# Optimization experiments

Hardware: AMD Instinct MI355X
Metric: run time of the kernel (lower is better)

## Reference

```python
import jax, jax.numpy as jnp
import numpy as np

K = 16          # n_neighbors
DS = 4          # downsampling_rate
EPS = 1e-5      # BatchNorm eps


def fps(pos, n_samples):
    """Farthest point sampling. pos: [N,3] -> [n_samples] int32 indices (start at node 0)."""
    N = pos.shape[0]
    def body(carry, _):
        dists, last = carry
        d = jnp.sum((pos - pos[last]) ** 2, axis=-1)
        dists = jnp.minimum(dists, d)
        nxt = jnp.argmax(dists).astype(jnp.int32)
        return (dists, nxt), nxt
    init = (jnp.full((N,), 1e10, dtype=pos.dtype), jnp.int32(0))
    _, idxs = jax.lax.scan(body, init, None, length=n_samples - 1)
    return jnp.concatenate([jnp.zeros((1,), jnp.int32), idxs])


def knn(pos, k):
    """k nearest neighbors (incl. self). pos: [N,3] -> [N,k] indices."""
    d = jnp.sum((pos[:, None, :] - pos[None, :, :]) ** 2, axis=-1)  # [N,N]
    _, idx = jax.lax.top_k(-d, k)
    return idx


def setup_inputs() -> dict:
    key = jax.random.key(0)
    ks = jax.random.split(key, 8)
    B, N, C = 4, 4096, 64
    sizes = [C + 3, 128, 128]
    inp = {
        "feat": jax.random.normal(ks[0], (B, N, C), jnp.float32),
        "pos": jax.random.normal(ks[1], (B, N, 3), jnp.float32),
    }
    for i in range(2):
        cin, cout = sizes[i], sizes[i + 1]
        inp[f"W{i+1}"] = jax.random.normal(ks[2 + 2 * i], (cout, cin), jnp.float32) / np.float32(np.sqrt(cin))
        inp[f"b{i+1}"] = jnp.zeros((cout,), jnp.float32)
        inp[f"gamma{i+1}"] = jnp.ones((cout,), jnp.float32)
        inp[f"beta{i+1}"] = jnp.zeros((cout,), jnp.float32)
    return inp


def reference(feat, pos, W1, b1, gamma1, beta1, W2, b2, gamma2, beta2):
    B, N, C = feat.shape
    n_samples = N // DS
    # FPS centroids; the torch code selects them via a boolean mask, i.e. ascending node order
    cent = jax.vmap(lambda p: fps(p, n_samples))(pos)          # [B,S]
    cent = jnp.sort(cent, axis=-1)
    # KNN graph per cloud
    nbr = jax.vmap(lambda p: knn(p, K))(pos)                    # [B,N,K]
    nbr_pos = jax.vmap(lambda p, i: p[i])(pos, nbr)             # [B,N,K,3]
    nbr_feat = jax.vmap(lambda f, i: f[i])(feat, nbr)           # [B,N,K,C]
    # RelativePositionMessage: concat(src_pos - dst_pos, src_feat)
    rel = nbr_pos - pos[:, :, None, :]
    h = jnp.concatenate([rel, nbr_feat], axis=-1)               # [B,N,K,C+3]
    # PointNetConv: (1x1 Conv2d -> BatchNorm2d(training stats) -> ReLU) x2, then max over neighbors
    for W, b, g, be in ((W1, b1, gamma1, beta1), (W2, b2, gamma2, beta2)):
        h = jnp.einsum('bnkc,dc->bnkd', h, W) + b
        mu = jnp.mean(h, axis=(0, 1, 2))
        var = jnp.var(h, axis=(0, 1, 2))
        h = (h - mu) * jax.lax.rsqrt(var + EPS) * g + be
        h = jax.nn.relu(h)
    new_feat = jnp.max(h, axis=2)                               # [B,N,Cout]
    # select centroid nodes
    pos_res = jnp.take_along_axis(pos, cent[..., None], axis=1)        # [B,S,3]
    feat_res = jnp.take_along_axis(new_feat, cent[..., None], axis=1)  # [B,S,Cout]
    return pos_res, feat_res
```

## Files before the change

### kernel.cpp

```cpp
#include <hip/hip_runtime.h>

typedef float f2 __attribute__((ext_vector_type(2)));

#define NB 4
#define NN 4096
#define KNB 16
#define NS 1024
#define M1TOT (NB*NN*KNB)
#define EPSBN 1e-5f
#define FPS_SPLIT 511
#define PADN 4124

__device__ __align__(16) float g_h1[(size_t)M1TOT*128];
__device__ __align__(16) int   g_nbr[NB*NN*KNB];
__device__ __align__(16) float g_fps_rd[NB][NN];
__device__ unsigned g_fps_sel[NB][256];
__device__ int   g_fps_last[NB];
__device__ int   g_cent[NB][NS];
__device__ float g_sum1[128], g_sq1[128], g_sum2[128], g_sq2[128];
__device__ __align__(16) float g_hminN[NB*NN*128];
__device__ __align__(16) float g_hmaxN[NB*NN*128];

struct __align__(16) FpsSm {
    float spx[NN], spy[NN], spz[NN];
    float sv[2][4]; int sj[2][4];
    int   cnts[256];
};
struct __align__(16) G1Sm {
    float  xls[64*68];
    float4 wlsA[68*16], wlsB[68*16];
    float  redS[512], redQ[512];
};
struct __align__(16) G2Sm {
    float  yls[64*132];
    float4 w2A[32*16], w2B[32*16];
    float  scs[128], shs[128];
    float  redS[512], redQ[512];
};
union KnnSm {
    struct { float spx[PADN], spy[PADN], spz[PADN]; } p;
    unsigned long long pairs[32*130];
};

__device__ __forceinline__ void fps_chunk(const float* __restrict__ pos, float* __restrict__ out,
                                          FpsSm* sm, int b, int t, int it0, int it1,
                                          bool first, bool last)
{
#pragma clang fp contract(off)
    const float* pb = pos + b*NN*3;
    for (int i = t; i < NN; i += 256) { sm->spx[i]=pb[3*i]; sm->spy[i]=pb[3*i+1]; sm->spz[i]=pb[3*i+2]; }
    __syncthreads();
    f2 rx[8], ry[8], rz[8], rd[8];
    #pragma unroll
    for (int p=0;p<8;p++){
        int j = (t<<4) + 2*p;
        rx[p] = *(const f2*)&sm->spx[j];
        ry[p] = *(const f2*)&sm->spy[j];
        rz[p] = *(const f2*)&sm->spz[j];
    }
    unsigned sel; int j2;
    if (first) {
        #pragma unroll
        for (int p=0;p<8;p++) rd[p] = (f2){1e10f, 1e10f};
        sel = (t==0) ? 1u : 0u;
        j2 = 0;
    } else {
        #pragma unroll
        for (int u=0;u<4;u++){
            float4 ld = *(const float4*)&g_fps_rd[b][(t<<4)+(u<<2)];
            rd[2*u]   = (f2){ld.x, ld.y};
            rd[2*u+1] = (f2){ld.z, ld.w};
        }
        sel = g_fps_sel[b][t];
        j2  = g_fps_last[b];
    }
    float cx = sm->spx[j2], cy = sm->spy[j2], cz = sm->spz[j2];

    for (int it = it0; it < it1; ++it) {
        const int par = it & 1;
        const f2 c2x = {cx,cx}, c2y = {cy,cy}, c2z = {cz,cz};
        #pragma unroll
        for (int p=0;p<8;p++){
            f2 dx = rx[p]-c2x, dy = ry[p]-c2y, dz = rz[p]-c2z;
            f2 m0 = dx*dx, m1 = dy*dy, m2 = dz*dz;
            f2 a0 = m0 + m1;
            f2 d  = a0 + m2;
            rd[p] = __builtin_elementwise_min(rd[p], d);
        }
        f2 t0 = __builtin_elementwise_max(rd[0], rd[1]);
        f2 t1 = __builtin_elementwise_max(rd[2], rd[3]);
        f2 t2 = __builtin_elementwise_max(rd[4], rd[5]);
        f2 t3 = __builtin_elementwise_max(rd[6], rd[7]);
        t0 = __builtin_elementwise_max(t0, t1);
        t2 = __builtin_elementwise_max(t2, t3);
        t0 = __builtin_elementwise_max(t0, t2);
        float wv = fmaxf(t0.x, t0.y);
        #pragma unroll
        for (int m=1;m<64;m<<=1) wv = fmaxf(wv, __shfl_xor(wv, m));
        int lj = 0x7fffffff;
        #pragma unroll
        for (int p=7;p>=0;p--){
            lj = (rd[p].y == wv) ? ((t<<4)+2*p+1) : lj;
            lj = (rd[p].x == wv) ? ((t<<4)+2*p)   : lj;
        }
        unsigned long long mk = __ballot(lj != 0x7fffffff);
        int src = __ffsll(mk) - 1;
        int bj = __shfl(lj, src);
        if ((t & 63) == 0) { sm->sv[par][t>>6] = wv; sm->sj[par][t>>6] = bj; }
        __syncthreads();
        float v = sm->sv[par][0]; int jn = sm->sj[par][0];
        #pragma unroll
        for (int w=1;w<4;w++){
            float ov = sm->sv[par][w]; int oj = sm->sj[par][w];
            if (ov > v || (ov == v && oj < jn)) { v = ov; jn = oj; }
        }
        j2 = jn;
        cx = sm->spx[j2]; cy = sm->spy[j2]; cz = sm->spz[j2];
        unsigned rel = (unsigned)(j2 - (t<<4));
        if (rel < 16u) sel |= (1u << rel);
    }

    if (!last) {
        #pragma unroll
        for (int u=0;u<4;u++){
            float4 st = {rd[2*u].x, rd[2*u].y, rd[2*u+1].x, rd[2*u+1].y};
            *(float4*)&g_fps_rd[b][(t<<4)+(u<<2)] = st;
        }
        g_fps_sel[b][t] = sel;
        if (t == 0) g_fps_last[b] = j2;
    } else {
        sm->cnts[t] = (int)__popc(sel);
        __syncthreads();
        if (t == 0) { int run = 0; for (int i=0;i<256;i++){ int c = sm->cnts[i]; sm->cnts[i] = run; run += c; } }
        __syncthreads();
        int base = sm->cnts[t];
        #pragma unroll
        for (int i=0;i<16;i++){
            int j = (t<<4)+i;
            if (sel & (1u<<i)) {
                g_cent[b][base] = j;
                float* po = out + (size_t)((b<<10)+base)*3;
                po[0]=sm->spx[j]; po[1]=sm->spy[j]; po[2]=sm->spz[j];
                base++;
            }
        }
    }
}

__device__ __forceinline__ void key_ins(unsigned long long (&kk)[16], unsigned long long &wmax,
                                        unsigned long long key)
{
    unsigned long long m0 = kk[0]; int mj = 0;
    #pragma unroll
    for (int u=1;u<16;u++){ if (kk[u] > m0){ m0 = kk[u]; mj = u; } }
    #pragma unroll
    for (int u=0;u<16;u++){ if (u == mj) kk[u] = key; }
    unsigned long long w = kk[0];
    #pragma unroll
    for (int u=1;u<16;u++) w = (kk[u] > w) ? kk[u] : w;
    wmax = w;
}

__global__ __launch_bounds__(256, 1) void kPre(const float* __restrict__ pos)
{
    __shared__ KnnSm sm;
    const int blk = blockIdx.x, t = threadIdx.x;
    if (blk >= 512) {
        if (t < 128) { g_sum1[t]=0.f; g_sq1[t]=0.f; g_sum2[t]=0.f; g_sq2[t]=0.f; }
        return;
    }
    const int b = blk >> 7;
    const int qloc = t >> 3, tq = t & 7;
    const int q = ((blk & 127) << 5) + qloc;
    const float* pb = pos + b*NN*3;
    for (int i = t; i < NN; i += 256) {
        int l = i + ((i >> 9) << 2);
        sm.p.spx[l]=pb[3*i]; sm.p.spy[l]=pb[3*i+1]; sm.p.spz[l]=pb[3*i+2];
    }
    __syncthreads();
    const int lq = q + ((q >> 9) << 2);
    const float qx = sm.p.spx[lq], qy = sm.p.spy[lq], qz = sm.p.spz[lq];
    float bd[16]; int bi[16];
    #pragma unroll
    for (int u=0;u<16;u++){ bd[u]=3e38f; bi[u]=0; }
    float wmax = 3e38f;
    const int base = tq * 516;
    const int j0 = tq << 9;
    for (int i = 0; i < 512; ++i) {
        float dx = sm.p.spx[base+i]-qx, dy = sm.p.spy[base+i]-qy, dz = sm.p.spz[base+i]-qz;
        float d = __fadd_rn(__fadd_rn(__fmul_rn(dx,dx),__fmul_rn(dy,dy)),__fmul_rn(dz,dz));
        if (d < wmax) {
            float m0 = bd[0]; int mj = 0;
            #pragma unroll
            for (int u=1;u<16;u++){ if (bd[u] > m0) { m0 = bd[u]; mj = u; } }
            #pragma unroll
            for (int u=0;u<16;u++){ if (u == mj) { bd[u] = d; bi[u] = j0 + i; } }
            wmax = bd[0];
            #pragma unroll
            for (int u=1;u<16;u++) wmax = fmaxf(wmax, bd[u]);
        }
    }
    __syncthreads();
    #pragma unroll
    for (int u=0;u<16;u++)
        sm.pairs[qloc*130 + (tq<<4) + u] =
            ((unsigned long long)__float_as_uint(bd[u]) << 32) | (unsigned)bi[u];
    __syncthreads();
    if (tq == 0) {
        unsigned long long kk2[16];
        #pragma unroll
        for (int u=0;u<16;u++) kk2[u] = ~0ULL;
        unsigned long long wm2 = ~0ULL;
        for (int e = 0; e < 128; ++e) {
            unsigned long long key = sm.pairs[qloc*130 + e];
            if (key < wm2) key_ins(kk2, wm2, key);
        }
        int* dst = g_nbr + ((size_t)(b*NN + q) << 4);
        #pragma unroll
        for (int u=0;u<16;u++) dst[u] = (int)(kk2[u] & 0xffffffffu);
    }
}

__global__ __launch_bounds__(256, 1) void kS1(const float* __restrict__ feat, const float* __restrict__ pos,
                                              const float* __restrict__ W1, const float* __restrict__ b1)
{
    __shared__ union { FpsSm f; G1Sm g; } sm;
    const int blk = blockIdx.x, t = threadIdx.x;
    if (blk < 4) { fps_chunk(pos, nullptr, &sm.f, blk, t, 0, FPS_SPLIT, true, false); return; }
    const int gb = blk - 4;
    const int b = gb >> 10, nb = (gb & 1023) << 2;

    for (int e = t; e < 128*67; e += 256) {
        int co = e / 67, ci = e - co*67;
        int row = (ci < 3) ? (64 + ci) : (ci - 3);
        int cgd = co >> 3, h = co & 7;
        float w = W1[e];
        if (h < 4) ((float*)&sm.g.wlsA[row*16 + cgd])[h]   = w;
        else       ((float*)&sm.g.wlsB[row*16 + cgd])[h-4] = w;
    }
    if (t < 64) { ((float*)&sm.g.wlsA[67*16])[t] = 0.f; ((float*)&sm.g.wlsB[67*16])[t] = 0.f; }
    {
        const int s = t >> 2, h = t & 3;
        const int n = nb + (s >> 4), k = s & 15;
        const int gq = b*NN + n;
        const int idx = g_nbr[(gq << 4) + k];
        const float* fr = feat + ((size_t)(b*NN + idx) << 6) + (h << 4);
        float* xr = sm.g.xls + s*68 + (h << 4);
        #pragma unroll
        for (int u=0;u<4;u++) ((float4*)xr)[u] = ((const float4*)fr)[u];
        if (h == 0) {
            const float* pn = pos + (size_t)gq*3;
            const float* pi = pos + (size_t)(b*NN + idx)*3;
            sm.g.xls[s*68 + 64] = pi[0]-pn[0];
            sm.g.xls[s*68 + 65] = pi[1]-pn[1];
            sm.g.xls[s*68 + 66] = pi[2]-pn[2];
            sm.g.xls[s*68 + 67] = 0.f;
        }
    }
    __syncthreads();
    const int cg = t & 15, sg = t >> 4, w = t >> 6;
    float acc[4][8];
    #pragma unroll
    for (int r=0;r<4;r++)
        #pragma unroll
        for (int c=0;c<8;c++) acc[r][c] = 0.f;
    for (int c4 = 0; c4 < 17; ++c4) {
        float4 wA[4], wB[4];
        #pragma unroll
        for (int ii=0;ii<4;ii++){ wA[ii] = sm.g.wlsA[(4*c4+ii)*16 + cg]; wB[ii] = sm.g.wlsB[(4*c4+ii)*16 + cg]; }
        #pragma unroll
        for (int r=0;r<4;r++){
            float4 xv = *(const float4*)&sm.g.xls[(sg + (r<<4))*68 + (c4<<2)];
            #pragma unroll
            for (int ii=0;ii<4;ii++){
                float x = (ii==0)?xv.x:(ii==1)?xv.y:(ii==2)?xv.z:xv.w;
                acc[r][0] = fmaf(x, wA[ii].x, acc[r][0]);
                acc[r][1] = fmaf(x, wA[ii].y, acc[r][1]);
                acc[r][2] = fmaf(x, wA[ii].z, acc[r][2]);
                acc[r][3] = fmaf(x, wA[ii].w, acc[r][3]);
                acc[r][4] = fmaf(x, wB[ii].x, acc[r][4]);
                acc[r][5] = fmaf(x, wB[ii].y, acc[r][5]);
                acc[r][6] = fmaf(x, wB[ii].z, acc[r][6]);
                acc[r][7] = fmaf(x, wB[ii].w, acc[r][7]);
            }
        }
    }
    float4 bA = *(const float4*)&b1[cg<<3];
    float4 bB = *(const float4*)&b1[(cg<<3)+4];
    float h1v[4][8];
    #pragma unroll
    for (int r=0;r<4;r++){
        h1v[r][0]=acc[r][0]+bA.x; h1v[r][1]=acc[r][1]+bA.y; h1v[r][2]=acc[r][2]+bA.z; h1v[r][3]=acc[r][3]+bA.w;
        h1v[r][4]=acc[r][4]+bB.x; h1v[r][5]=acc[r][5]+bB.y; h1v[r][6]=acc[r][6]+bB.z; h1v[r][7]=acc[r][7]+bB.w;
    }
    #pragma unroll
    for (int c=0;c<8;c++){
        const int ch = (cg<<3)+c;
        float ls=0.f, lq=0.f;
        #pragma unroll
        for (int r=0;r<4;r++){ float h1 = h1v[r][c]; ls += h1; lq = fmaf(h1,h1,lq); }
        ls += __shfl_xor(ls,16); ls += __shfl_xor(ls,32);
        lq += __shfl_xor(lq,16); lq += __shfl_xor(lq,32);
        if ((sg & 3) == 0) { sm.g.redS[w*128 + ch] = ls; sm.g.redQ[w*128 + ch] = lq; }
    }
    #pragma unroll
    for (int r=0;r<4;r++){
        const int gs = (b*NN + nb + r)*16 + sg;
        float4 o0 = {h1v[r][0],h1v[r][1],h1v[r][2],h1v[r][3]};
        float4 o1 = {h1v[r][4],h1v[r][5],h1v[r][6],h1v[r][7]};
        *(float4*)&g_h1[(size_t)gs*128 + (cg<<3)]     = o0;
        *(float4*)&g_h1[(size_t)gs*128 + (cg<<3) + 4] = o1;
    }
    __syncthreads();
    if (t < 128) {
        float s = sm.g.redS[t] + sm.g.redS[128+t] + sm.g.redS[256+t] + sm.g.redS[384+t];
        float q = sm.g.redQ[t] + sm.g.redQ[128+t] + sm.g.redQ[256+t] + sm.g.redQ[384+t];
        atomicAdd(&g_sum1[t], s);
        atomicAdd(&g_sq1[t], q);
    }
}

__global__ __launch_bounds__(256, 1) void kS2(const float* __restrict__ pos, float* __restrict__ out,
        const float* __restrict__ W2, const float* __restrict__ b2,
        const float* __restrict__ gamma1, const float* __restrict__ beta1)
{
    __shared__ union { FpsSm f; G2Sm g; } sm;
    const int blk = blockIdx.x, t = threadIdx.x;
    if (blk < 4) { fps_chunk(pos, out, &sm.f, blk, t, FPS_SPLIT, NS-1, false, true); return; }
    const int gb = blk - 4;
    const int b = gb >> 10, nb = (gb & 1023) << 2;
    if (t < 128) {
        const float inv = 1.f/(float)M1TOT;
        float mu  = g_sum1[t]*inv;
        float var = g_sq1[t]*inv - mu*mu;
        float sc  = gamma1[t]*rsqrtf(var + EPSBN);
        sm.g.scs[t] = sc; sm.g.shs[t] = beta1[t] - mu*sc;
    }
    __syncthreads();
    {
        const float* hsrc = g_h1 + (size_t)((b*NN + nb)*16)*128;
        const int ch0 = (4*t) & 127;
        float4 sc4 = *(const float4*)&sm.g.scs[ch0];
        float4 sh4 = *(const float4*)&sm.g.shs[ch0];
        #pragma unroll
        for (int j=0;j<8;j++){
            int f = j*1024 + 4*t;
            float4 v = *(const float4*)&hsrc[f];
            int s = f >> 7;
            float4 yv;
            yv.x = fmaxf(0.f, fmaf(v.x, sc4.x, sh4.x));
            yv.y = fmaxf(0.f, fmaf(v.y, sc4.y, sh4.y));
            yv.z = fmaxf(0.f, fmaf(v.z, sc4.z, sh4.z));
            yv.w = fmaxf(0.f, fmaf(v.w, sc4.w, sh4.w));
            *(float4*)&sm.g.yls[s*132 + ch0] = yv;
        }
    }
    const int cg = t & 15, sg = t >> 4, w = t >> 6;
    float acc2[4][8];
    #pragma unroll
    for (int r=0;r<4;r++)
        #pragma unroll
        for (int c=0;c<8;c++) acc2[r][c]=0.f;
    for (int kc = 0; kc < 4; ++kc) {
        for (int e = t; e < 4096; e += 256) {
            int d = e >> 5, kk = e & 31;
            float wv = W2[(d << 7) + (kc<<5) + kk];
            int cgd = d >> 3, h = d & 7;
            if (h < 4) ((float*)&sm.g.w2A[kk*16 + cgd])[h]   = wv;
            else       ((float*)&sm.g.w2B[kk*16 + cgd])[h-4] = wv;
        }
        __syncthreads();
        #pragma unroll
        for (int c4=0;c4<8;c4++){
            float4 wA[4], wB[4];
            #pragma unroll
            for (int ii=0;ii<4;ii++){ wA[ii] = sm.g.w2A[(4*c4+ii)*16 + cg]; wB[ii] = sm.g.w2B[(4*c4+ii)*16 + cg]; }
            #pragma unroll
            for (int r=0;r<4;r++){
                float4 yv = *(const float4*)&sm.g.yls[((sg<<2)+r)*132 + (kc<<5) + (c4<<2)];
                #pragma unroll
                for (int ii=0;ii<4;ii++){
                    float y = (ii==0)?yv.x:(ii==1)?yv.y:(ii==2)?yv.z:yv.w;
                    acc2[r][0] = fmaf(y, wA[ii].x, acc2[r][0]);
                    acc2[r][1] = fmaf(y, wA[ii].y, acc2[r][1]);
                    acc2[r][2] = fmaf(y, wA[ii].z, acc2[r][2]);
                    acc2[r][3] = fmaf(y, wA[ii].w, acc2[r][3]);
                    acc2[r][4] = fmaf(y, wB[ii].x, acc2[r][4]);
                    acc2[r][5] = fmaf(y, wB[ii].y, acc2[r][5]);
                    acc2[r][6] = fmaf(y, wB[ii].z, acc2[r][6]);
                    acc2[r][7] = fmaf(y, wB[ii].w, acc2[r][7]);
                }
            }
        }
        __syncthreads();
    }
    const int node = nb + (sg >> 2);
    #pragma unroll
    for (int c=0;c<8;c++){
        const int ch = (cg<<3)+c;
        const float bb = b2[ch];
        float ls=0.f, lq=0.f, mn=3e38f, mx=-3e38f;
        #pragma unroll
        for (int r=0;r<4;r++){
            float h2 = acc2[r][c] + bb;
            ls += h2; lq = fmaf(h2,h2,lq);
            mn = fminf(mn,h2); mx = fmaxf(mx,h2);
        }
        ls += __shfl_xor(ls,16); ls += __shfl_xor(ls,32);
        lq += __shfl_xor(lq,16); lq += __shfl_xor(lq,32);
        if ((sg & 3) == 0) { sm.g.redS[w*128 + ch] = ls; sm.g.redQ[w*128 + ch] = lq; }
        float o;
        o = __shfl_xor(mn,16); mn = fminf(mn,o);
        o = __shfl_xor(mn,32); mn = fminf(mn,o);
        o = __shfl_xor(mx,16); mx = fmaxf(mx,o);
        o = __shfl_xor(mx,32); mx = fmaxf(mx,o);
        if ((sg & 3) == 0) {
            const int oo = ((b<<12)+node)*128 + ch;
            g_hminN[oo] = mn; g_hmaxN[oo] = mx;
        }
    }
    __syncthreads();
    if (t < 128) {
        float s = sm.g.redS[t] + sm.g.redS[128+t] + sm.g.redS[256+t] + sm.g.redS[384+t];
        float q = sm.g.redQ[t] + sm.g.redQ[128+t] + sm.g.redQ[256+t] + sm.g.redQ[384+t];
        atomicAdd(&g_sum2[t], s);
        atomicAdd(&g_sq2[t], q);
    }
}

__global__ __launch_bounds__(256) void kFinal(const float* __restrict__ gamma2, const float* __restrict__ beta2,
                                              float* __restrict__ out)
{
    const int gid = blockIdx.x*256 + threadIdx.x;
    const int base = gid << 2;
    const int sl = base >> 7;
    const int b = sl >> 10, slot = sl & 1023;
    const int ch0 = base & 127;
    const int node = g_cent[b][slot];
    const int src = ((b<<12)+node)*128 + ch0;
    const float inv = 1.f/(float)M1TOT;
    float4 mx = *(const float4*)&g_hmaxN[src];
    float4 mn = *(const float4*)&g_hminN[src];
    float4 o;
    #pragma unroll
    for (int c=0;c<4;c++){
        int ch = ch0 + c;
        float mu = g_sum2[ch]*inv, var = g_sq2[ch]*inv - mu*mu;
        float sc = gamma2[ch]*rsqrtf(var+EPSBN), sh = beta2[ch] - mu*sc;
        float hi = (c==0)?mx.x:(c==1)?mx.y:(c==2)?mx.z:mx.w;
        float lo = (c==0)?mn.x:(c==1)?mn.y:(c==2)?mn.z:mn.w;
        float v = fmaxf(0.f, fmaf((sc >= 0.f) ? hi : lo, sc, sh));
        if (c==0) o.x=v; else if (c==1) o.y=v; else if (c==2) o.z=v; else o.w=v;
    }
    *(float4*)&out[12288 + base] = o;
}

extern "C" void kernel_launch(void* const* d_in, const int* in_sizes, int n_in,
                              void* d_out, int out_size, void* d_ws, size_t ws_size,
                              hipStream_t stream)
{
    (void)in_sizes; (void)n_in; (void)d_ws; (void)ws_size; (void)out_size;
    const float* feat = (const float*)d_in[0];
    const float* pos  = (const float*)d_in[1];
    const float* W1   = (const float*)d_in[2];
    const float* b1   = (const float*)d_in[3];
    const float* g1   = (const float*)d_in[4];
    const float* be1  = (const float*)d_in[5];
    const float* W2   = (const float*)d_in[6];
    const float* b2   = (const float*)d_in[7];
    const float* g2   = (const float*)d_in[8];
    const float* be2  = (const float*)d_in[9];
    float* out = (float*)d_out;

    kPre  <<<dim3(513),  dim3(256), 0, stream>>>(pos);
    kS1   <<<dim3(4100), dim3(256), 0, stream>>>(feat, pos, W1, b1);
    kS2   <<<dim3(4100), dim3(256), 0, stream>>>(pos, out, W2, b2, g1, be1);
    kFinal<<<dim3(512),  dim3(256), 0, stream>>>(g2, be2, out);
}
```

Before: 1.470 ms.

## Recompute first pointwise conv in second pass instead of materializing h1

Removes the global g_h1 intermediate (one value per sample per channel, over 128 MB). The second-stage kernel now re-does the neighbor gather and the first GEMM before applying BatchNorm1 and ReLU. The first-stage kernel only accumulates the BatchNorm statistics. This trades a large write-then-read of HBM for redundant gather and GEMM work, and the shared-memory layout is unified into one scratch buffer. The benefit may be hidden if the FPS blocks that share these launches are the critical path.

```diff
diff --git a/kernel.cpp b/kernel.cpp
--- a/kernel.cpp
+++ b/kernel.cpp
@@ -11,7 +11,6 @@
 #define FPS_SPLIT 511
 #define PADN 4124
 
-__device__ __align__(16) float g_h1[(size_t)M1TOT*128];
 __device__ __align__(16) int   g_nbr[NB*NN*KNB];
 __device__ __align__(16) float g_fps_rd[NB][NN];
 __device__ unsigned g_fps_sel[NB][256];
@@ -27,15 +26,13 @@
     int   cnts[256];
 };
 struct __align__(16) G1Sm {
-    float  xls[64*68];
-    float4 wlsA[68*16], wlsB[68*16];
-    float  redS[512], redQ[512];
+    float sb[13056];
+    float redS[512], redQ[512];
 };
 struct __align__(16) G2Sm {
-    float  yls[64*132];
-    float4 w2A[32*16], w2B[32*16];
-    float  scs[128], shs[128];
-    float  redS[512], redQ[512];
+    float sb[13056];
+    float scs[128], shs[128];
+    float redS[512], redQ[512];
 };
 union KnnSm {
     struct { float spx[PADN], spy[PADN], spz[PADN]; } p;
@@ -221,45 +218,42 @@
     }
 }
 
-__global__ __launch_bounds__(256, 1) void kS1(const float* __restrict__ feat, const float* __restrict__ pos,
-                                              const float* __restrict__ W1, const float* __restrict__ b1)
-{
-    __shared__ union { FpsSm f; G1Sm g; } sm;
-    const int blk = blockIdx.x, t = threadIdx.x;
-    if (blk < 4) { fps_chunk(pos, nullptr, &sm.f, blk, t, 0, FPS_SPLIT, true, false); return; }
-    const int gb = blk - 4;
-    const int b = gb >> 10, nb = (gb & 1023) << 2;
-
-    for (int e = t; e < 128*67; e += 256) {
-        int co = e / 67, ci = e - co*67;
-        int row = (ci < 3) ? (64 + ci) : (ci - 3);
-        int cgd = co >> 3, h = co & 7;
-        float w = W1[e];
-        if (h < 4) ((float*)&sm.g.wlsA[row*16 + cgd])[h]   = w;
-        else       ((float*)&sm.g.wlsB[row*16 + cgd])[h-4] = w;
-    }
-    if (t < 64) { ((float*)&sm.g.wlsA[67*16])[t] = 0.f; ((float*)&sm.g.wlsB[67*16])[t] = 0.f; }
+__device__ __forceinline__ void w1_gather_gemm1(const float* __restrict__ feat,
+        const float* __restrict__ pos, const float* __restrict__ W1,
+        float* __restrict__ sb, int b, int nb, int t, float acc[4][8])
+{
+    float* wAf = sb + 4352;
+    float* wBf = sb + 8704;
+    for (int a = t; a < 4352; a += 256) {
+        int row = a >> 6, cgd = (a >> 2) & 15, h = a & 3;
+        int coA = (cgd << 3) + h;
+        int ci  = (row < 64) ? (row + 3) : (row - 64);
+        float vA = (row < 67) ? W1[coA * 67 + ci] : 0.f;
+        float vB = (row < 67) ? W1[(coA + 4) * 67 + ci] : 0.f;
+        wAf[a] = vA; wBf[a] = vB;
+    }
     {
         const int s = t >> 2, h = t & 3;
         const int n = nb + (s >> 4), k = s & 15;
         const int gq = b*NN + n;
         const int idx = g_nbr[(gq << 4) + k];
         const float* fr = feat + ((size_t)(b*NN + idx) << 6) + (h << 4);
-        float* xr = sm.g.xls + s*68 + (h << 4);
+        float* xr = sb + s*68 + (h << 4);
         #pragma unroll
         for (int u=0;u<4;u++) ((float4*)xr)[u] = ((const float4*)fr)[u];
         if (h == 0) {
             const float* pn = pos + (size_t)gq*3;
             const float* pi = pos + (size_t)(b*NN + idx)*3;
-            sm.g.xls[s*68 + 64] = pi[0]-pn[0];
-            sm.g.xls[s*68 + 65] = pi[1]-pn[1];
-            sm.g.xls[s*68 + 66] = pi[2]-pn[2];
-            sm.g.xls[s*68 + 67] = 0.f;
-        }
-    }
-    __syncthreads();
-    const int cg = t & 15, sg = t >> 4, w = t >> 6;
-    float acc[4][8];
+            sb[s*68 + 64] = pi[0]-pn[0];
+            sb[s*68 + 65] = pi[1]-pn[1];
+            sb[s*68 + 66] = pi[2]-pn[2];
+            sb[s*68 + 67] = 0.f;
+        }
+    }
+    __syncthreads();
+    const int cg = t & 15, sg = t >> 4;
+    const float4* wA4 = (const float4*)wAf;
+    const float4* wB4 = (const float4*)wBf;
     #pragma unroll
     for (int r=0;r<4;r++)
         #pragma unroll
@@ -267,10 +261,10 @@
     for (int c4 = 0; c4 < 17; ++c4) {
         float4 wA[4], wB[4];
         #pragma unroll
-        for (int ii=0;ii<4;ii++){ wA[ii] = sm.g.wlsA[(4*c4+ii)*16 + cg]; wB[ii] = sm.g.wlsB[(4*c4+ii)*16 + cg]; }
+        for (int ii=0;ii<4;ii++){ wA[ii] = wA4[(4*c4+ii)*16 + cg]; wB[ii] = wB4[(4*c4+ii)*16 + cg]; }
         #pragma unroll
         for (int r=0;r<4;r++){
-            float4 xv = *(const float4*)&sm.g.xls[(sg + (r<<4))*68 + (c4<<2)];
+            float4 xv = *(const float4*)&sb[(sg + (r<<4))*68 + (c4<<2)];
             #pragma unroll
             for (int ii=0;ii<4;ii++){
                 float x = (ii==0)?xv.x:(ii==1)?xv.y:(ii==2)?xv.z:xv.w;
@@ -285,31 +279,32 @@
             }
         }
     }
+}
+
+__global__ __launch_bounds__(256, 1) void kS1(const float* __restrict__ feat, const float* __restrict__ pos,
+                                              const float* __restrict__ W1, const float* __restrict__ b1)
+{
+    __shared__ union { FpsSm f; G1Sm g; } sm;
+    const int blk = blockIdx.x, t = threadIdx.x;
+    if (blk < 4) { fps_chunk(pos, nullptr, &sm.f, blk, t, 0, FPS_SPLIT, true, false); return; }
+    const int gb = blk - 4;
+    const int b = gb >> 10, nb = (gb & 1023) << 2;
+    float acc[4][8];
+    w1_gather_gemm1(feat, pos, W1, sm.g.sb, b, nb, t, acc);
+    const int cg = t & 15, sg = t >> 4, w = t >> 6;
     float4 bA = *(const float4*)&b1[cg<<3];
     float4 bB = *(const float4*)&b1[(cg<<3)+4];
-    float h1v[4][8];
-    #pragma unroll
-    for (int r=0;r<4;r++){
-        h1v[r][0]=acc[r][0]+bA.x; h1v[r][1]=acc[r][1]+bA.y; h1v[r][2]=acc[r][2]+bA.z; h1v[r][3]=acc[r][3]+bA.w;
-        h1v[r][4]=acc[r][4]+bB.x; h1v[r][5]=acc[r][5]+bB.y; h1v[r][6]=acc[r][6]+bB.z; h1v[r][7]=acc[r][7]+bB.w;
-    }
     #pragma unroll
     for (int c=0;c<8;c++){
         const int ch = (cg<<3)+c;
+        const float bb = (c<4) ? ((c==0)?bA.x:(c==1)?bA.y:(c==2)?bA.z:bA.w)
+                               : ((c==4)?bB.x:(c==5)?bB.y:(c==6)?bB.z:bB.w);
         float ls=0.f, lq=0.f;
         #pragma unroll
-        for (int r=0;r<4;r++){ float h1 = h1v[r][c]; ls += h1; lq = fmaf(h1,h1,lq); }
+        for (int r=0;r<4;r++){ float h1 = acc[r][c] + bb; ls += h1; lq = fmaf(h1,h1,lq); }
         ls += __shfl_xor(ls,16); ls += __shfl_xor(ls,32);
         lq += __shfl_xor(lq,16); lq += __shfl_xor(lq,32);
         if ((sg & 3) == 0) { sm.g.redS[w*128 + ch] = ls; sm.g.redQ[w*128 + ch] = lq; }
-    }
-    #pragma unroll
-    for (int r=0;r<4;r++){
-        const int gs = (b*NN + nb + r)*16 + sg;
-        float4 o0 = {h1v[r][0],h1v[r][1],h1v[r][2],h1v[r][3]};
-        float4 o1 = {h1v[r][4],h1v[r][5],h1v[r][6],h1v[r][7]};
-        *(float4*)&g_h1[(size_t)gs*128 + (cg<<3)]     = o0;
-        *(float4*)&g_h1[(size_t)gs*128 + (cg<<3) + 4] = o1;
     }
     __syncthreads();
     if (t < 128) {
@@ -320,9 +315,10 @@
     }
 }
 
-__global__ __launch_bounds__(256, 1) void kS2(const float* __restrict__ pos, float* __restrict__ out,
-        const float* __restrict__ W2, const float* __restrict__ b2,
-        const float* __restrict__ gamma1, const float* __restrict__ beta1)
+__global__ __launch_bounds__(256, 1) void kS2(const float* __restrict__ feat, const float* __restrict__ pos,
+        float* __restrict__ out, const float* __restrict__ W1, const float* __restrict__ b1,
+        const float* __restrict__ gamma1, const float* __restrict__ beta1,
+        const float* __restrict__ W2, const float* __restrict__ b2)
 {
     __shared__ union { FpsSm f; G2Sm g; } sm;
     const int blk = blockIdx.x, t = threadIdx.x;
@@ -336,48 +332,58 @@
         float sc  = gamma1[t]*rsqrtf(var + EPSBN);
         sm.g.scs[t] = sc; sm.g.shs[t] = beta1[t] - mu*sc;
     }
+    float acc[4][8];
+    w1_gather_gemm1(feat, pos, W1, sm.g.sb, b, nb, t, acc);
+    const int cg = t & 15, sg = t >> 4, w = t >> 6;
     __syncthreads();
     {
-        const float* hsrc = g_h1 + (size_t)((b*NN + nb)*16)*128;
-        const int ch0 = (4*t) & 127;
-        float4 sc4 = *(const float4*)&sm.g.scs[ch0];
-        float4 sh4 = *(const float4*)&sm.g.shs[ch0];
-        #pragma unroll
-        for (int j=0;j<8;j++){
-            int f = j*1024 + 4*t;
-            float4 v = *(const float4*)&hsrc[f];
-            int s = f >> 7;
-            float4 yv;
-            yv.x = fmaxf(0.f, fmaf(v.x, sc4.x, sh4.x));
-            yv.y = fmaxf(0.f, fmaf(v.y, sc4.y, sh4.y));
-            yv.z = fmaxf(0.f, fmaf(v.z, sc4.z, sh4.z));
-            yv.w = fmaxf(0.f, fmaf(v.w, sc4.w, sh4.w));
-            *(float4*)&sm.g.yls[s*132 + ch0] = yv;
-        }
-    }
-    const int cg = t & 15, sg = t >> 4, w = t >> 6;
+        float4 bA = *(const float4*)&b1[cg<<3];
+        float4 bB = *(const float4*)&b1[(cg<<3)+4];
+        float4 scA = *(const float4*)&sm.g.scs[cg<<3];
+        float4 scB = *(const float4*)&sm.g.scs[(cg<<3)+4];
+        float4 shA = *(const float4*)&sm.g.shs[cg<<3];
+        float4 shB = *(const float4*)&sm.g.shs[(cg<<3)+4];
+        #pragma unroll
+        for (int r=0;r<4;r++){
+            const int s = sg + (r<<4);
+            float4 y0, y1;
+            y0.x = fmaxf(0.f, fmaf(acc[r][0]+bA.x, scA.x, shA.x));
+            y0.y = fmaxf(0.f, fmaf(acc[r][1]+bA.y, scA.y, shA.y));
+            y0.z = fmaxf(0.f, fmaf(acc[r][2]+bA.z, scA.z, shA.z));
+            y0.w = fmaxf(0.f, fmaf(acc[r][3]+bA.w, scA.w, shA.w));
+            y1.x = fmaxf(0.f, fmaf(acc[r][4]+bB.x, scB.x, shB.x));
+            y1.y = fmaxf(0.f, fmaf(acc[r][5]+bB.y, scB.y, shB.y));
+            y1.z = fmaxf(0.f, fmaf(acc[r][6]+bB.z, scB.z, shB.z));
+            y1.w = fmaxf(0.f, fmaf(acc[r][7]+bB.w, scB.w, shB.w));
+            *(float4*)&sm.g.sb[s*132 + (cg<<3)]     = y0;
+            *(float4*)&sm.g.sb[s*132 + (cg<<3) + 4] = y1;
+        }
+    }
+    float* w2Af = sm.g.sb + 8448;
+    float* w2Bf = sm.g.sb + 10496;
     float acc2[4][8];
     #pragma unroll
     for (int r=0;r<4;r++)
         #pragma unroll
         for (int c=0;c<8;c++) acc2[r][c]=0.f;
     for (int kc = 0; kc < 4; ++kc) {
-        for (int e = t; e < 4096; e += 256) {
-            int d = e >> 5, kk = e & 31;
-            float wv = W2[(d << 7) + (kc<<5) + kk];
-            int cgd = d >> 3, h = d & 7;
-            if (h < 4) ((float*)&sm.g.w2A[kk*16 + cgd])[h]   = wv;
-            else       ((float*)&sm.g.w2B[kk*16 + cgd])[h-4] = wv;
+        for (int a = t; a < 2048; a += 256) {
+            int kk = a >> 6, cgd = (a >> 2) & 15, h = a & 3;
+            int dA = (cgd << 3) + h;
+            w2Af[a] = W2[(dA << 7) + (kc << 5) + kk];
+            w2Bf[a] = W2[((dA + 4) << 7) + (kc << 5) + kk];
         }
         __syncthreads();
+        const float4* w2A4 = (const float4*)w2Af;
+        const float4* w2B4 = (const float4*)w2Bf;
         #pragma unroll
         for (int c4=0;c4<8;c4++){
             float4 wA[4], wB[4];
             #pragma unroll
-            for (int ii=0;ii<4;ii++){ wA[ii] = sm.g.w2A[(4*c4+ii)*16 + cg]; wB[ii] = sm.g.w2B[(4*c4+ii)*16 + cg]; }
+            for (int ii=0;ii<4;ii++){ wA[ii] = w2A4[(4*c4+ii)*16 + cg]; wB[ii] = w2B4[(4*c4+ii)*16 + cg]; }
             #pragma unroll
             for (int r=0;r<4;r++){
-                float4 yv = *(const float4*)&sm.g.yls[((sg<<2)+r)*132 + (kc<<5) + (c4<<2)];
+                float4 yv = *(const float4*)&sm.g.sb[((sg<<2)+r)*132 + (kc<<5) + (c4<<2)];
                 #pragma unroll
                 for (int ii=0;ii<4;ii++){
                     float y = (ii==0)?yv.x:(ii==1)?yv.y:(ii==2)?yv.z:yv.w;
@@ -474,6 +480,6 @@
 
     kPre  <<<dim3(513),  dim3(256), 0, stream>>>(pos);
     kS1   <<<dim3(4100), dim3(256), 0, stream>>>(feat, pos, W1, b1);
-    kS2   <<<dim3(4100), dim3(256), 0, stream>>>(pos, out, W2, b2, g1, be1);
+    kS2   <<<dim3(4100), dim3(256), 0, stream>>>(feat, pos, out, W1, b1, g1, be1, W2, b2);
     kFinal<<<dim3(512),  dim3(256), 0, stream>>>(g2, be2, out);
 }
```

After: 1.427 ms. 2.9% less time.
